# Kernel tuning notes

Hardware: AMD Instinct MI355X
Metric: run time of the kernel (lower is better)

## Reference

```python
import jax, jax.numpy as jnp
import numpy as np
import math

B, S, D, H = 2, 2048, 1024, 16
DH = D // H
MASK_VALUE = -1e6


def setup_inputs() -> dict:
    key = jax.random.key(0)
    ks = jax.random.split(key, 6)
    x = jax.random.normal(ks[0], (B, S, D), dtype=jnp.float32)
    scale = 1.0 / math.sqrt(D)
    Wq = jax.random.normal(ks[1], (D, D), dtype=jnp.float32) * scale
    Wk = jax.random.normal(ks[2], (D, D), dtype=jnp.float32) * scale
    Wv = jax.random.normal(ks[3], (D, D), dtype=jnp.float32) * scale
    Wo = jax.random.normal(ks[4], (D, D), dtype=jnp.float32) * scale
    valid_lens = jax.random.randint(ks[5], (B,), 1, S + 1, dtype=jnp.int32)
    return {"x": x, "Wq": Wq, "Wk": Wk, "Wv": Wv, "Wo": Wo, "valid_lens": valid_lens}


def reference(x, Wq, Wk, Wv, Wo, valid_lens):
    # Projections (Linear with bias=False): [B,S,D] -> split into H heads of DH
    def split_heads(y):
        return y.reshape(B, S, H, DH).transpose(0, 2, 1, 3)  # [B,H,S,DH]

    q = split_heads(x @ Wq)
    k = split_heads(x @ Wk)
    v = split_heads(x @ Wv)

    # scores [B,H,Sq,Sk]; masking depends only on key position per batch
    scores = jnp.einsum("bhqd,bhkd->bhqk", q, k) / math.sqrt(DH)
    key_pos = jnp.arange(S, dtype=jnp.int32)  # [Sk]
    mask = key_pos[None, None, None, :] < valid_lens[:, None, None, None]
    scores = jnp.where(mask, scores, MASK_VALUE)
    attn = jax.nn.softmax(scores, axis=-1)  # dropout is identity in eval

    out = jnp.einsum("bhqk,bhkd->bhqd", attn, v)  # [B,H,S,DH]
    out = out.transpose(0, 2, 1, 3).reshape(B, S, D)  # concat heads
    return out @ Wo
```

## Files before the change

kernel.cpp:

```cpp
#include <hip/hip_runtime.h>

#define Bdim 2
#define Sdim 2048
#define Ddim 1024
#define Hdim 16

typedef unsigned short u16;
typedef u16 u16x8 __attribute__((ext_vector_type(8)));
typedef u16 u16x4 __attribute__((ext_vector_type(4)));
typedef unsigned u32x4 __attribute__((ext_vector_type(4)));
typedef __bf16 bf16x8 __attribute__((ext_vector_type(8)));
typedef float f32x4 __attribute__((ext_vector_type(4)));
typedef float f32x16 __attribute__((ext_vector_type(16)));

static __device__ __forceinline__ u16 f2bf(float f) {
  unsigned u = __float_as_uint(f);
  u += 0x7fffu + ((u >> 16) & 1u);
  return (u16)(u >> 16);
}
static __device__ __forceinline__ float bf2f(u16 v) {
  return __uint_as_float((unsigned)v << 16);
}
static __device__ __forceinline__ bf16x8 asbf(u16x8 v) {
  return __builtin_bit_cast(bf16x8, v);
}
static __device__ __forceinline__ f32x4 mfma16(bf16x8 a, bf16x8 b, f32x4 c) {
  return __builtin_amdgcn_mfma_f32_16x16x32_bf16(a, b, c, 0, 0, 0);
}
static __device__ __forceinline__ f32x16 mfma32(bf16x8 a, bf16x8 b, f32x16 c) {
  return __builtin_amdgcn_mfma_f32_32x32x16_bf16(a, b, c, 0, 0, 0);
}

static __device__ __forceinline__ size_t tcell(int R, int k) {
  return ((size_t)(R >> 7) * 16 + (k >> 6)) * 1024 + (R & 127) * 8 + ((k >> 3) & 7);
}

__global__ __launch_bounds__(256) void cvtx(const float* __restrict__ x,
                                            u16* __restrict__ xt) {
  int i = blockIdx.x * 256 + threadIdx.x;
  const float4* xp = (const float4*)x;
  float4 a = xp[2 * i], b = xp[2 * i + 1];
  u16x8 o;
  o[0] = f2bf(a.x); o[1] = f2bf(a.y); o[2] = f2bf(a.z); o[3] = f2bf(a.w);
  o[4] = f2bf(b.x); o[5] = f2bf(b.y); o[6] = f2bf(b.z); o[7] = f2bf(b.w);
  int R = i >> 7, k = (i & 127) * 8;
  ((u16x8*)xt)[tcell(R, k)] = o;
}

__global__ __launch_bounds__(256) void transw(
    const float* __restrict__ W0, const float* __restrict__ W1,
    const float* __restrict__ W2, const float* __restrict__ W3,
    u16* __restrict__ T0, u16* __restrict__ T1,
    u16* __restrict__ T2, u16* __restrict__ T3) {
  const float* W = blockIdx.z == 0 ? W0 : blockIdx.z == 1 ? W1 : blockIdx.z == 2 ? W2 : W3;
  u16* T = blockIdx.z == 0 ? T0 : blockIdx.z == 1 ? T1 : blockIdx.z == 2 ? T2 : T3;
  __shared__ float tile[32][33];
  const int t = threadIdx.x;
  const int k0 = blockIdx.x * 32, n0 = blockIdx.y * 32;
  const int r = t >> 3, cq = (t & 7) * 4;
  float4 v = *(const float4*)(W + (size_t)(k0 + r) * Ddim + n0 + cq);
  tile[r][cq] = v.x; tile[r][cq + 1] = v.y; tile[r][cq + 2] = v.z; tile[r][cq + 3] = v.w;
  __syncthreads();
  u16x4 ov;
  ov[0] = f2bf(tile[cq][r]);
  ov[1] = f2bf(tile[cq + 1][r]);
  ov[2] = f2bf(tile[cq + 2][r]);
  ov[3] = f2bf(tile[cq + 3][r]);
  int n = n0 + r, k = k0 + cq;
  *(u16x4*)(T + tcell(n, k) * 8 + (k & 7)) = ov;
}

__global__ __launch_bounds__(256) void vtrans(const u16* __restrict__ V,
                                              u16* __restrict__ Vt) {
  __shared__ u16 tile[32][72];
  const int t = threadIdx.x;
  const int s0 = blockIdx.x * 32;
  const int bh = blockIdx.y, b = bh >> 4, h = bh & 15;
  {
    int sl = t >> 3, dq = (t & 7) * 8;
    u16x8 v = *(const u16x8*)(V + (size_t)(b * Sdim + s0 + sl) * Ddim + h * 64 + dq);
    *(u16x8*)(&tile[sl][dq]) = v;
  }
  __syncthreads();
  {
    int dl = t >> 2, sq = (t & 3) * 8;
    u16x8 v;
#pragma unroll
    for (int i = 0; i < 8; i++) v[i] = tile[sq + i][dl];
    int s = s0 + sq;
    int kt = s >> 6, c = (s >> 3) & 7;
    *(u16x8*)(Vt + ((((size_t)bh * 32 + kt) * 8 + c) * 64 + dl) * 8) = v;
  }
}

__global__ __launch_bounds__(256) void tilek(const u16* __restrict__ K,
                                             u16* __restrict__ Kt) {
  int tid = blockIdx.x * 256 + threadIdx.x;
  int row = tid & 63;
  int c = (tid >> 6) & 7;
  int kt = (tid >> 9) & 31;
  int bh = tid >> 14;
  int b = bh >> 4, h = bh & 15;
  u16x8 kc = *(const u16x8*)(K + (size_t)(b * Sdim + kt * 64 + row) * Ddim + h * 64 + c * 8);
  ((u16x8*)Kt)[tid] = kc;
}

template <bool F32OUT>
__global__ __launch_bounds__(256) void gemm128(
    const u16* __restrict__ A,
    const u16* __restrict__ Bt0, const u16* __restrict__ Bt1, const u16* __restrict__ Bt2,
    void* __restrict__ C0v, void* __restrict__ C1v, void* __restrict__ C2v) {
  __shared__ u16 As[128 * 64];
  __shared__ u16 Bs[128 * 64];
  const int zz = blockIdx.y >> 3;
  const u16* Bt = (zz == 0) ? Bt0 : (zz == 1) ? Bt1 : Bt2;
  void* Cv = (zz == 0) ? C0v : (zz == 1) ? C1v : C2v;

  const int t = threadIdx.x;
  const int lane = t & 63, w = t >> 6;
  const int wm = w >> 1, wn = w & 1;
  const int c = lane & 15, g = lane >> 4;
  const int mb = blockIdx.x, nb = blockIdx.y & 7;
  const float oscale = (!F32OUT && zz == 0) ? 0.125f : 1.0f;

  const f32x4 zv = {0.f, 0.f, 0.f, 0.f};
  f32x4 acc[4][4];
#pragma unroll
  for (int m = 0; m < 4; m++)
#pragma unroll
    for (int n = 0; n < 4; n++) acc[m][n] = zv;

  const u16x8* Ac = (const u16x8*)A;
  const u16x8* Bc = (const u16x8*)Bt;
  u16x8 ra[4], rb[4];
#pragma unroll
  for (int i = 0; i < 4; i++) {
    ra[i] = Ac[(size_t)(mb * 16 + 0) * 1024 + t + 256 * i];
    rb[i] = Bc[(size_t)(nb * 16 + 0) * 1024 + t + 256 * i];
  }
#pragma unroll
  for (int i = 0; i < 4; i++) {
    int idx = t + 256 * i;
    int row = idx >> 3, ch = idx & 7;
    int sw = (ch ^ (row & 7)) * 8;
    *(u16x8*)(As + row * 64 + sw) = ra[i];
    *(u16x8*)(Bs + row * 64 + sw) = rb[i];
  }
  __syncthreads();

  for (int kt = 0; kt < 16; ++kt) {
    const bool more = (kt + 1) < 16;
    if (more) {
#pragma unroll
      for (int i = 0; i < 4; i++) {
        ra[i] = Ac[(size_t)(mb * 16 + kt + 1) * 1024 + t + 256 * i];
        rb[i] = Bc[(size_t)(nb * 16 + kt + 1) * 1024 + t + 256 * i];
      }
    }
#pragma unroll
    for (int kh = 0; kh < 2; kh++) {
      bf16x8 af[4], bfr[4];
#pragma unroll
      for (int m = 0; m < 4; m++) {
        int row = wm * 64 + m * 16 + c;
        int chr = kh * 4 + g;
        af[m] = asbf(*(const u16x8*)(As + row * 64 + ((chr ^ (row & 7)) * 8)));
      }
#pragma unroll
      for (int n = 0; n < 4; n++) {
        int row = wn * 64 + n * 16 + c;
        int chr = kh * 4 + g;
        bfr[n] = asbf(*(const u16x8*)(Bs + row * 64 + ((chr ^ (row & 7)) * 8)));
      }
#pragma unroll
      for (int m = 0; m < 4; m++)
#pragma unroll
        for (int n = 0; n < 4; n++) acc[m][n] = mfma16(af[m], bfr[n], acc[m][n]);
    }
    if (more) {
      __syncthreads();
#pragma unroll
      for (int i = 0; i < 4; i++) {
        int idx = t + 256 * i;
        int row = idx >> 3, ch = idx & 7;
        int sw = (ch ^ (row & 7)) * 8;
        *(u16x8*)(As + row * 64 + sw) = ra[i];
        *(u16x8*)(Bs + row * 64 + sw) = rb[i];
      }
      __syncthreads();
    }
  }
#pragma unroll
  for (int m = 0; m < 4; m++)
#pragma unroll
    for (int n = 0; n < 4; n++)
#pragma unroll
      for (int r = 0; r < 4; r++) {
        int row = mb * 128 + wm * 64 + m * 16 + 4 * g + r;
        int col = nb * 128 + wn * 64 + n * 16 + c;
        if (F32OUT)
          ((float*)Cv)[(size_t)row * 1024 + col] = acc[m][n][r];
        else
          ((u16*)Cv)[(size_t)row * 1024 + col] = f2bf(acc[m][n][r] * oscale);
      }
}

__global__ __launch_bounds__(256) void gemm_wo(
    const u16* __restrict__ A, const u16* __restrict__ Bt, float* __restrict__ C) {
  __shared__ u16 As[64 * 64];
  __shared__ u16 Bs[128 * 64];
  const int t = threadIdx.x;
  const int lane = t & 63, w = t >> 6;
  const int wm = w >> 1, wn = w & 1;
  const int c = lane & 15, g = lane >> 4;
  const int mb = blockIdx.x, nb = blockIdx.y;

  const f32x4 zv = {0.f, 0.f, 0.f, 0.f};
  f32x4 acc[2][4];
#pragma unroll
  for (int m = 0; m < 2; m++)
#pragma unroll
    for (int n = 0; n < 4; n++) acc[m][n] = zv;

  const u16x8* Ac = (const u16x8*)A;
  const u16x8* Bc = (const u16x8*)Bt;
  const size_t abase = (size_t)(mb >> 1) * 16384 + (size_t)(mb & 1) * 512;
  u16x8 ra[2], rb[4];
#pragma unroll
  for (int i = 0; i < 2; i++) ra[i] = Ac[abase + 0 * 1024 + t + 256 * i];
#pragma unroll
  for (int i = 0; i < 4; i++) rb[i] = Bc[(size_t)(nb * 16 + 0) * 1024 + t + 256 * i];
  {
#pragma unroll
    for (int i = 0; i < 2; i++) {
      int idx = t + 256 * i;
      int row = idx >> 3, ch = idx & 7;
      *(u16x8*)(As + row * 64 + ((ch ^ (row & 7)) * 8)) = ra[i];
    }
#pragma unroll
    for (int i = 0; i < 4; i++) {
      int idx = t + 256 * i;
      int row = idx >> 3, ch = idx & 7;
      *(u16x8*)(Bs + row * 64 + ((ch ^ (row & 7)) * 8)) = rb[i];
    }
  }
  __syncthreads();

  for (int kt = 0; kt < 16; ++kt) {
    const bool more = (kt + 1) < 16;
    if (more) {
#pragma unroll
      for (int i = 0; i < 2; i++) ra[i] = Ac[abase + (size_t)(kt + 1) * 1024 + t + 256 * i];
#pragma unroll
      for (int i = 0; i < 4; i++)
        rb[i] = Bc[(size_t)(nb * 16 + kt + 1) * 1024 + t + 256 * i];
    }
#pragma unroll
    for (int kh = 0; kh < 2; kh++) {
      bf16x8 af[2], bfr[4];
#pragma unroll
      for (int m = 0; m < 2; m++) {
        int row = wm * 32 + m * 16 + c;
        int chr = kh * 4 + g;
        af[m] = asbf(*(const u16x8*)(As + row * 64 + ((chr ^ (row & 7)) * 8)));
      }
#pragma unroll
      for (int n = 0; n < 4; n++) {
        int row = wn * 64 + n * 16 + c;
        int chr = kh * 4 + g;
        bfr[n] = asbf(*(const u16x8*)(Bs + row * 64 + ((chr ^ (row & 7)) * 8)));
      }
#pragma unroll
      for (int m = 0; m < 2; m++)
#pragma unroll
        for (int n = 0; n < 4; n++) acc[m][n] = mfma16(af[m], bfr[n], acc[m][n]);
    }
    if (more) {
      __syncthreads();
#pragma unroll
      for (int i = 0; i < 2; i++) {
        int idx = t + 256 * i;
        int row = idx >> 3, ch = idx & 7;
        *(u16x8*)(As + row * 64 + ((ch ^ (row & 7)) * 8)) = ra[i];
      }
#pragma unroll
      for (int i = 0; i < 4; i++) {
        int idx = t + 256 * i;
        int row = idx >> 3, ch = idx & 7;
        *(u16x8*)(Bs + row * 64 + ((ch ^ (row & 7)) * 8)) = rb[i];
      }
      __syncthreads();
    }
  }
#pragma unroll
  for (int m = 0; m < 2; m++)
#pragma unroll
    for (int n = 0; n < 4; n++)
#pragma unroll
      for (int r = 0; r < 4; r++) {
        int row = mb * 64 + wm * 32 + m * 16 + 4 * g + r;
        int col = nb * 128 + wn * 64 + n * 16 + c;
        C[(size_t)row * 1024 + col] = acc[m][n][r];
      }
}

__global__ __launch_bounds__(64, 4) void attn_kernel(
    const u16* __restrict__ Q, const u16* __restrict__ Kt,
    const u16* __restrict__ Vt, const int* __restrict__ vlen,
    u16* __restrict__ O, u16* __restrict__ Opart, float2* __restrict__ mlp) {
  __shared__ u16 ot[32][72];
  const int lane = threadIdx.x;
  const int q = lane & 31, hi = lane >> 5;
  const int bh = blockIdx.y, b = bh >> 4, h = bh & 15;
  const int q0 = blockIdx.x * 32;
  const int nv = vlen[b];
  const int NS = gridDim.z, z = blockIdx.z;

  bf16x8 qf[4];
  {
    const u16* qp = Q + (size_t)(b * Sdim + q0 + q) * Ddim + h * 64 + hi * 8;
#pragma unroll
    for (int s = 0; s < 4; s++) qf[s] = asbf(*(const u16x8*)(qp + s * 16));
  }

  f32x16 o0, o1;
#pragma unroll
  for (int r = 0; r < 16; r++) { o0[r] = 0.f; o1[r] = 0.f; }
  float m = -3.0e38f, l = 0.f;

  const int nt = (nv + 63) >> 6;
  const int chunk = (nt + NS - 1) / NS;
  const int t0 = z * chunk;
  const int t1 = min(nt, t0 + chunk);
  for (int kt = t0; kt < t1; ++kt) {
    const int k0 = kt * 64;
    const u16* Ktile = Kt + ((size_t)bh * 32 + kt) * 4096;
    const u16* Vtile = Vt + ((size_t)bh * 32 + kt) * 4096;
    f32x16 sc[2];
#pragma unroll
    for (int kb = 0; kb < 2; kb++) {
      f32x16 acc;
#pragma unroll
      for (int r = 0; r < 16; r++) acc[r] = 0.f;
#pragma unroll
      for (int s = 0; s < 4; s++) {
        bf16x8 kf = asbf(*(const u16x8*)(Ktile + (2 * s + hi) * 512 + (kb * 32 + q) * 8));
        acc = mfma32(kf, qf[s], acc);
      }
      sc[kb] = acc;
    }
    if (k0 + 64 > nv) {
#pragma unroll
      for (int kb = 0; kb < 2; kb++)
#pragma unroll
        for (int r = 0; r < 16; r++) {
          int key = k0 + kb * 32 + (r & 3) + 8 * (r >> 2) + 4 * hi;
          if (key >= nv) sc[kb][r] = -1e30f;
        }
    }
    float mx[16];
#pragma unroll
    for (int r = 0; r < 16; r++) mx[r] = fmaxf(sc[0][r], sc[1][r]);
#pragma unroll
    for (int st = 8; st > 0; st >>= 1)
#pragma unroll
      for (int r = 0; r < st; r++) mx[r] = fmaxf(mx[r], mx[r + st]);
    float tm = fmaxf(mx[0], __shfl_xor(mx[0], 32));
    if (!__all(tm <= m + 8.f)) {
      float mn = fmaxf(m, tm);
      float al = __expf(m - mn);
#pragma unroll
      for (int r = 0; r < 16; r++) { o0[r] *= al; o1[r] *= al; }
      l *= al;
      m = mn;
    }
    unsigned pw[4][4];
    float s0 = 0.f, s1 = 0.f, s2 = 0.f, s3 = 0.f;
#pragma unroll
    for (int kb = 0; kb < 2; kb++)
#pragma unroll
      for (int hh = 0; hh < 2; hh++)
#pragma unroll
        for (int wi = 0; wi < 4; wi++) {
          float e0 = __expf(sc[kb][hh * 8 + wi * 2] - m);
          float e1 = __expf(sc[kb][hh * 8 + wi * 2 + 1] - m);
          if (wi == 0) s0 += e0 + e1;
          else if (wi == 1) s1 += e0 + e1;
          else if (wi == 2) s2 += e0 + e1;
          else s3 += e0 + e1;
          asm("v_cvt_pk_bf16_f32 %0, %1, %2"
              : "=v"(pw[kb * 2 + hh][wi]) : "v"(e0), "v"(e1));
        }
    float ssum = (s0 + s1) + (s2 + s3);
    ssum += __shfl_xor(ssum, 32);
    l += ssum;
#pragma unroll
    for (int f = 0; f < 4; f++) {
      asm("v_permlane32_swap_b32 %0, %1" : "+v"(pw[f][0]), "+v"(pw[f][2]));
      asm("v_permlane32_swap_b32 %0, %1" : "+v"(pw[f][1]), "+v"(pw[f][3]));
    }
#pragma unroll
    for (int f = 0; f < 4; f++) {
      u32x4 wv = {pw[f][0], pw[f][1], pw[f][2], pw[f][3]};
      bf16x8 pa = __builtin_bit_cast(bf16x8, wv);
      bf16x8 va = asbf(*(const u16x8*)(Vtile + (2 * f + hi) * 512 + q * 8));
      bf16x8 vb = asbf(*(const u16x8*)(Vtile + (2 * f + hi) * 512 + (32 + q) * 8));
      o0 = mfma32(va, pa, o0);
      o1 = mfma32(vb, pa, o1);
    }
  }
  const float scale = (NS == 1) ? (1.f / l) : 1.f;
#pragma unroll
  for (int r = 0; r < 16; r++) {
    const int dh = (r & 3) + 8 * (r >> 2) + 4 * hi;
    ot[q][dh] = f2bf(o0[r] * scale);
    ot[q][32 + dh] = f2bf(o1[r] * scale);
  }
  asm volatile("s_waitcnt lgkmcnt(0)" ::: "memory");
  __builtin_amdgcn_sched_barrier(0);
  if (NS == 1) {
    int R = b * Sdim + q0 + q;
    size_t cellbase = ((size_t)(R >> 7) * 16 + h) * 1024 + (R & 127) * 8 + hi * 4;
#pragma unroll
    for (int j = 0; j < 4; j++)
      ((u16x8*)O)[cellbase + j] = *(const u16x8*)(&ot[q][hi * 32 + j * 8]);
  } else {
    u16* op = Opart + ((size_t)(z * 32 + bh) * Sdim + q0 + q) * 64 + hi * 32;
#pragma unroll
    for (int j = 0; j < 4; j++)
      *(u16x8*)(op + j * 8) = *(const u16x8*)(&ot[q][hi * 32 + j * 8]);
    if (hi == 0)
      mlp[(size_t)(z * 32 + bh) * Sdim + q0 + q] = make_float2(m, l);
  }
}

template <int NS>
__global__ __launch_bounds__(256) void attn_combine(
    const u16* __restrict__ Opart, const float2* __restrict__ mlp,
    u16* __restrict__ O) {
  const int t = threadIdx.x;
  const int bh = blockIdx.y, b = bh >> 4, h = bh & 15;
  const int q = blockIdx.x * 32 + (t >> 3);
  const int d0 = (t & 7) * 8;
  float2 ml[NS];
  float M = -3.0e38f;
#pragma unroll
  for (int z = 0; z < NS; z++) {
    ml[z] = mlp[(size_t)(z * 32 + bh) * Sdim + q];
    M = fmaxf(M, ml[z].x);
  }
  float acc[8];
#pragma unroll
  for (int i = 0; i < 8; i++) acc[i] = 0.f;
  float wsum = 0.f;
#pragma unroll
  for (int z = 0; z < NS; z++) {
    float w = __expf(ml[z].x - M);
    wsum += w * ml[z].y;
    u16x8 ov = *(const u16x8*)(Opart + ((size_t)(z * 32 + bh) * Sdim + q) * 64 + d0);
#pragma unroll
    for (int i = 0; i < 8; i++) acc[i] += w * bf2f(ov[i]);
  }
  const float inv = 1.f / wsum;
  u16x8 res;
#pragma unroll
  for (int i = 0; i < 8; i++) res[i] = f2bf(acc[i] * inv);
  int R = b * Sdim + q;
  ((u16x8*)O)[((size_t)(R >> 7) * 16 + h) * 1024 + (R & 127) * 8 + (d0 >> 3)] = res;
}

extern "C" void kernel_launch(void* const* d_in, const int* in_sizes, int n_in,
                              void* d_out, int out_size, void* d_ws, size_t ws_size,
                              hipStream_t stream) {
  const float* x = (const float*)d_in[0];
  const float* Wq = (const float*)d_in[1];
  const float* Wk = (const float*)d_in[2];
  const float* Wv = (const float*)d_in[3];
  const float* Wo = (const float*)d_in[4];
  const int* vl = (const int*)d_in[5];
  float* out = (float*)d_out;

  char* ws = (char*)d_ws;
  const size_t SZ_X = (size_t)Bdim * Sdim * Ddim * sizeof(u16);
  const size_t SZ_W = (size_t)Ddim * Ddim * sizeof(u16);
  u16* xt = (u16*)ws; ws += SZ_X;
  u16* WqT = (u16*)ws; ws += SZ_W;
  u16* WkT = (u16*)ws; ws += SZ_W;
  u16* WvT = (u16*)ws; ws += SZ_W;
  u16* WoT = (u16*)ws; ws += SZ_W;
  u16* Qb = (u16*)ws; ws += SZ_X;
  u16* Kb = (u16*)ws; ws += SZ_X;
  u16* Vb = (u16*)ws; ws += SZ_X;
  u16* Obt = (u16*)ws; ws += SZ_X;
  u16* Ktb = (u16*)ws; ws += SZ_X;
  u16* Vtb = (u16*)ws; ws += SZ_X;

  const size_t PER_SPLIT = (size_t)Bdim * Hdim * Sdim * 64 * sizeof(u16) +
                           (size_t)Bdim * Hdim * Sdim * sizeof(float2);
  size_t used = (size_t)(ws - (char*)d_ws);
  size_t avail = (ws_size > used) ? ws_size - used : 0;
  int NS = (avail >= 4 * PER_SPLIT) ? 4 : (avail >= 2 * PER_SPLIT) ? 2 : 1;
  u16* Opart = (u16*)ws;
  float2* mlp = (float2*)(ws + (size_t)NS * Bdim * Hdim * Sdim * 64 * sizeof(u16));

  cvtx<<<dim3((Bdim * Sdim * Ddim) / (8 * 256)), 256, 0, stream>>>(x, xt);
  transw<<<dim3(32, 32, 4), 256, 0, stream>>>(Wq, Wk, Wv, Wo, WqT, WkT, WvT, WoT);
  gemm128<false><<<dim3(32, 24), 256, 0, stream>>>(xt, WqT, WkT, WvT, Qb, Kb, Vb);
  vtrans<<<dim3(Sdim / 32, Bdim * Hdim), 256, 0, stream>>>(Vb, Vtb);
  tilek<<<dim3((Bdim * Sdim * Ddim / 8) / 256), 256, 0, stream>>>(Kb, Ktb);
  attn_kernel<<<dim3(Sdim / 32, Bdim * Hdim, NS), 64, 0, stream>>>(Qb, Ktb, Vtb, vl, Obt,
                                                                   Opart, mlp);
  if (NS == 4)
    attn_combine<4><<<dim3(Sdim / 32, Bdim * Hdim), 256, 0, stream>>>(Opart, mlp, Obt);
  else if (NS == 2)
    attn_combine<2><<<dim3(Sdim / 32, Bdim * Hdim), 256, 0, stream>>>(Opart, mlp, Obt);
  gemm_wo<<<dim3(64, 8), 256, 0, stream>>>(Obt, WoT, out);
}
```

Baseline: 119.3 us.

## Fuse K/V tiling and V transpose into QKV GEMM epilogue

The QKV projection GEMM now writes Q and K directly in the attention kernel's tiled layout and V in its transposed tile layout. This removes the separate vtrans and tilek kernels, along with their extra global read/write passes and launches. The attention kernel now loads Q from the tiled layout. The trade-off is that Q and K epilogue stores become scattered 2-byte writes at a stride of 8 elements, which may coalesce less well than the previous row-major stores.

```diff
diff --git a/kernel.cpp b/kernel.cpp
--- a/kernel.cpp
+++ b/kernel.cpp
@@ -70,58 +70,21 @@
   *(u16x4*)(T + tcell(n, k) * 8 + (k & 7)) = ov;
 }
 
-__global__ __launch_bounds__(256) void vtrans(const u16* __restrict__ V,
-                                              u16* __restrict__ Vt) {
-  __shared__ u16 tile[32][72];
-  const int t = threadIdx.x;
-  const int s0 = blockIdx.x * 32;
-  const int bh = blockIdx.y, b = bh >> 4, h = bh & 15;
-  {
-    int sl = t >> 3, dq = (t & 7) * 8;
-    u16x8 v = *(const u16x8*)(V + (size_t)(b * Sdim + s0 + sl) * Ddim + h * 64 + dq);
-    *(u16x8*)(&tile[sl][dq]) = v;
-  }
-  __syncthreads();
-  {
-    int dl = t >> 2, sq = (t & 3) * 8;
-    u16x8 v;
-#pragma unroll
-    for (int i = 0; i < 8; i++) v[i] = tile[sq + i][dl];
-    int s = s0 + sq;
-    int kt = s >> 6, c = (s >> 3) & 7;
-    *(u16x8*)(Vt + ((((size_t)bh * 32 + kt) * 8 + c) * 64 + dl) * 8) = v;
-  }
-}
-
-__global__ __launch_bounds__(256) void tilek(const u16* __restrict__ K,
-                                             u16* __restrict__ Kt) {
-  int tid = blockIdx.x * 256 + threadIdx.x;
-  int row = tid & 63;
-  int c = (tid >> 6) & 7;
-  int kt = (tid >> 9) & 31;
-  int bh = tid >> 14;
-  int b = bh >> 4, h = bh & 15;
-  u16x8 kc = *(const u16x8*)(K + (size_t)(b * Sdim + kt * 64 + row) * Ddim + h * 64 + c * 8);
-  ((u16x8*)Kt)[tid] = kc;
-}
-
-template <bool F32OUT>
-__global__ __launch_bounds__(256) void gemm128(
+__global__ __launch_bounds__(256) void gemm_qkv(
     const u16* __restrict__ A,
     const u16* __restrict__ Bt0, const u16* __restrict__ Bt1, const u16* __restrict__ Bt2,
-    void* __restrict__ C0v, void* __restrict__ C1v, void* __restrict__ C2v) {
+    u16* __restrict__ Qt, u16* __restrict__ Kt, u16* __restrict__ Vt) {
   __shared__ u16 As[128 * 64];
   __shared__ u16 Bs[128 * 64];
   const int zz = blockIdx.y >> 3;
   const u16* Bt = (zz == 0) ? Bt0 : (zz == 1) ? Bt1 : Bt2;
-  void* Cv = (zz == 0) ? C0v : (zz == 1) ? C1v : C2v;
 
   const int t = threadIdx.x;
   const int lane = t & 63, w = t >> 6;
   const int wm = w >> 1, wn = w & 1;
   const int c = lane & 15, g = lane >> 4;
   const int mb = blockIdx.x, nb = blockIdx.y & 7;
-  const float oscale = (!F32OUT && zz == 0) ? 0.125f : 1.0f;
+  const float oscale = (zz == 0) ? 0.125f : 1.0f;
 
   const f32x4 zv = {0.f, 0.f, 0.f, 0.f};
   f32x4 acc[4][4];
@@ -190,19 +153,35 @@
       __syncthreads();
     }
   }
-#pragma unroll
-  for (int m = 0; m < 4; m++)
-#pragma unroll
-    for (int n = 0; n < 4; n++)
-#pragma unroll
-      for (int r = 0; r < 4; r++) {
-        int row = mb * 128 + wm * 64 + m * 16 + 4 * g + r;
+  if (zz < 2) {
+    u16* Ct = (zz == 0) ? Qt : Kt;
+#pragma unroll
+    for (int m = 0; m < 4; m++)
+#pragma unroll
+      for (int n = 0; n < 4; n++) {
         int col = nb * 128 + wn * 64 + n * 16 + c;
-        if (F32OUT)
-          ((float*)Cv)[(size_t)row * 1024 + col] = acc[m][n][r];
-        else
-          ((u16*)Cv)[(size_t)row * 1024 + col] = f2bf(acc[m][n][r] * oscale);
-      }
+        int Rb = mb * 128 + wm * 64 + m * 16 + 4 * g;
+        size_t base = ((size_t)((Rb >> 11) * 16 + (col >> 6)) * 32 + ((Rb >> 6) & 31)) * 4096 +
+                      ((col & 63) >> 3) * 512 + (size_t)(Rb & 63) * 8 + (col & 7);
+#pragma unroll
+        for (int r = 0; r < 4; r++)
+          Ct[base + (size_t)r * 8] = f2bf(acc[m][n][r] * oscale);
+      }
+  } else {
+#pragma unroll
+    for (int m = 0; m < 4; m++)
+#pragma unroll
+      for (int n = 0; n < 4; n++) {
+        int col = nb * 128 + wn * 64 + n * 16 + c;
+        int Rb = mb * 128 + wm * 64 + m * 16 + 4 * g;
+        u16x4 ov;
+#pragma unroll
+        for (int r = 0; r < 4; r++) ov[r] = f2bf(acc[m][n][r]);
+        size_t addr = ((size_t)((Rb >> 11) * 16 + (col >> 6)) * 32 + ((Rb >> 6) & 31)) * 4096 +
+                      ((Rb & 63) >> 3) * 512 + (size_t)(col & 63) * 8 + (Rb & 7);
+        *(u16x4*)(Vt + addr) = ov;
+      }
+  }
 }
 
 __global__ __launch_bounds__(256) void gemm_wo(
@@ -305,7 +284,7 @@
 }
 
 __global__ __launch_bounds__(64, 4) void attn_kernel(
-    const u16* __restrict__ Q, const u16* __restrict__ Kt,
+    const u16* __restrict__ Qt, const u16* __restrict__ Kt,
     const u16* __restrict__ Vt, const int* __restrict__ vlen,
     u16* __restrict__ O, u16* __restrict__ Opart, float2* __restrict__ mlp) {
   __shared__ u16 ot[32][72];
@@ -318,9 +297,11 @@
 
   bf16x8 qf[4];
   {
-    const u16* qp = Q + (size_t)(b * Sdim + q0 + q) * Ddim + h * 64 + hi * 8;
-#pragma unroll
-    for (int s = 0; s < 4; s++) qf[s] = asbf(*(const u16x8*)(qp + s * 16));
+    const u16* Qtile = Qt + ((size_t)bh * 32 + (q0 >> 6)) * 4096;
+    int qrow = (q0 & 63) + q;
+#pragma unroll
+    for (int s = 0; s < 4; s++)
+      qf[s] = asbf(*(const u16x8*)(Qtile + (2 * s + hi) * 512 + qrow * 8));
   }
 
   f32x16 o0, o1;
@@ -488,12 +469,10 @@
   u16* WkT = (u16*)ws; ws += SZ_W;
   u16* WvT = (u16*)ws; ws += SZ_W;
   u16* WoT = (u16*)ws; ws += SZ_W;
-  u16* Qb = (u16*)ws; ws += SZ_X;
-  u16* Kb = (u16*)ws; ws += SZ_X;
-  u16* Vb = (u16*)ws; ws += SZ_X;
-  u16* Obt = (u16*)ws; ws += SZ_X;
+  u16* Qtb = (u16*)ws; ws += SZ_X;
   u16* Ktb = (u16*)ws; ws += SZ_X;
   u16* Vtb = (u16*)ws; ws += SZ_X;
+  u16* Obt = (u16*)ws; ws += SZ_X;
 
   const size_t PER_SPLIT = (size_t)Bdim * Hdim * Sdim * 64 * sizeof(u16) +
                            (size_t)Bdim * Hdim * Sdim * sizeof(float2);
@@ -505,10 +484,8 @@
 
   cvtx<<<dim3((Bdim * Sdim * Ddim) / (8 * 256)), 256, 0, stream>>>(x, xt);
   transw<<<dim3(32, 32, 4), 256, 0, stream>>>(Wq, Wk, Wv, Wo, WqT, WkT, WvT, WoT);
-  gemm128<false><<<dim3(32, 24), 256, 0, stream>>>(xt, WqT, WkT, WvT, Qb, Kb, Vb);
-  vtrans<<<dim3(Sdim / 32, Bdim * Hdim), 256, 0, stream>>>(Vb, Vtb);
-  tilek<<<dim3((Bdim * Sdim * Ddim / 8) / 256), 256, 0, stream>>>(Kb, Ktb);
-  attn_kernel<<<dim3(Sdim / 32, Bdim * Hdim, NS), 64, 0, stream>>>(Qb, Ktb, Vtb, vl, Obt,
+  gemm_qkv<<<dim3(32, 24), 256, 0, stream>>>(xt, WqT, WkT, WvT, Qtb, Ktb, Vtb);
+  attn_kernel<<<dim3(Sdim / 32, Bdim * Hdim, NS), 64, 0, stream>>>(Qtb, Ktb, Vtb, vl, Obt,
                                                                    Opart, mlp);
   if (NS == 4)
     attn_combine<4><<<dim3(Sdim / 32, Bdim * Hdim), 256, 0, stream>>>(Opart, mlp, Obt);
```

New measurement: 109.3 us. 1.09x faster.
